# Kernel tuning notes

Measured on AMD Instinct MI355X. Metric: run time of the kernel, lower is better.

The kernel has to match this reference:

```python
import jax, jax.numpy as jnp
import numpy as np


def setup_inputs() -> dict:
    key = jax.random.key(0)
    k1, k2, k3 = jax.random.split(key, 3)
    B, S, H, D, W = 2, 2048, 16, 128, 4  # W = world_size (ring steps); k,v carry W*S total KV
    q = jax.random.normal(k1, (B, S, H, D), dtype=jnp.float32)
    k = jax.random.normal(k2, (B, W * S, H, D), dtype=jnp.float32)
    v = jax.random.normal(k3, (B, W * S, H, D), dtype=jnp.float32)
    return {"q": q, "k": k, "v": v}


def _ring_attention(q, k, v):
    # q: [B,S,H,D]; k,v: [B,W*S,H,D] -- W ring steps over KV chunks of length S
    B, S, H, D = q.shape
    W = k.shape[1] // S
    scale = D ** -0.5
    kc = k.reshape(B, W, S, H, D).transpose(1, 0, 2, 3, 4)  # [W,B,S,H,D]
    vc = v.reshape(B, W, S, H, D).transpose(1, 0, 2, 3, 4)
    o0 = jnp.zeros((B, H, S, D), q.dtype)
    l0 = jnp.zeros((B, H, S, 1), q.dtype)
    m0 = jnp.full((B, H, S, 1), -jnp.inf, q.dtype)

    def step(carry, kv):
        o, l, m = carry
        kb, vb = kv  # [B,S,H,D]
        scores = jnp.einsum('bqhd,bkhd->bhqk', q, kb) * scale  # [B,H,S,S]
        m_blk = jnp.max(scores, axis=-1, keepdims=True)
        p = jnp.exp(scores - m_blk)
        l_blk = jnp.sum(p, axis=-1, keepdims=True)
        m_new = jnp.maximum(m, m_blk)
        alpha = jnp.exp(m - m_blk * 0 - m_new) if False else jnp.exp(m - m_new)
        beta = jnp.exp(m_blk - m_new)
        l_new = alpha * l + beta * l_blk
        o_blk = jnp.einsum('bhqk,bkhd->bhqd', p, vb)
        o_new = (alpha * o * l + beta * o_blk) / l_new  # online-softmax rescale (same as torch code)
        return (o_new, l_new, m_new), None

    (o, l, m), _ = jax.lax.scan(step, (o0, l0, m0), (kc, vc))
    return o.transpose(0, 2, 1, 3)  # back to [B,S,H,D]


def reference(q, k, v):
    return _ring_attention(q, k, v)
```

## Files before the change

### kernel.cpp

```cpp
#include <hip/hip_runtime.h>

namespace {
constexpr int Bc  = 2;
constexpr int Sq  = 2048;
constexpr int Hn  = 16;
constexpr int Dd  = 128;
constexpr int Skv = 8192;
constexpr int TK  = 64;
constexpr int NT  = Skv / TK;
constexpr int QT  = 256;
constexpr int PP  = 72;
constexpr int TILE_ELEMS = TK * Dd;
constexpr int QTF = 128;
constexpr int KPF = 136;
constexpr float C_EXP = (float)(0.08838834764831845 * 1.4426950408889634);
}

typedef __attribute__((ext_vector_type(8))) short short8;
typedef __attribute__((ext_vector_type(8))) unsigned short us8;
typedef __attribute__((ext_vector_type(4))) float f32x4;
typedef __attribute__((ext_vector_type(4))) unsigned short us4;

__device__ __forceinline__ unsigned short f2bf(float f) {
  unsigned int u = __builtin_bit_cast(unsigned int, f);
  u += 0x7fffu + ((u >> 16) & 1u);
  return (unsigned short)(u >> 16);
}

__device__ __forceinline__ void gload16(const unsigned short* g, unsigned short* l) {
  __builtin_amdgcn_global_load_lds(
      (__attribute__((address_space(1))) void*)(g),
      (__attribute__((address_space(3))) void*)(l), 16, 0, 0);
}

__global__ __launch_bounds__(256) void convert_kernel(
    const float* __restrict__ kg, const float* __restrict__ vg,
    unsigned short* __restrict__ kws, unsigned short* __restrict__ vws) {
  const int t = threadIdx.x;
  const int bid = blockIdx.x;
  const int bh = bid >> 7;
  const int tile = bid & 127;
  const int b = bh >> 4, h = bh & (Hn - 1);
  const size_t HD = (size_t)Hn * Dd;

  const float* kin = kg + ((size_t)b * Skv + (size_t)tile * TK) * HD + (size_t)h * Dd;
  const float* vin = vg + ((size_t)b * Skv + (size_t)tile * TK) * HD + (size_t)h * Dd;
  unsigned short* kout = kws + (size_t)bid * TILE_ELEMS;
  unsigned short* vout = vws + (size_t)bid * TILE_ELEMS;

  {
    const int key = t >> 2;
    const float* krow = kin + (size_t)key * HD;
    unsigned short* orow = kout + key * Dd;
#pragma unroll
    for (int i = 0; i < 4; ++i) {
      const int dblk = (t & 3) * 4 + i;
      const int dsrc = dblk ^ (key & 7);
      float4 a = *(const float4*)(krow + dsrc * 8);
      float4 c = *(const float4*)(krow + dsrc * 8 + 4);
      us8 w;
      w[0] = f2bf(a.x); w[1] = f2bf(a.y); w[2] = f2bf(a.z); w[3] = f2bf(a.w);
      w[4] = f2bf(c.x); w[5] = f2bf(c.y); w[6] = f2bf(c.z); w[7] = f2bf(c.w);
      *(us8*)&orow[dblk * 8] = w;
    }
  }

  {
    const int kblk = t & 7;
    const int d4 = t >> 3;
#pragma unroll
    for (int eh = 0; eh < 2; ++eh) {
      const int f = (2 * d4 + eh) & 7;
      const int sb = kblk ^ f;
      us8 w0, w1;
#pragma unroll
      for (int r = 0; r < 8; ++r) {
        const float* vp = vin + (size_t)(sb * 8 + r) * HD + d4 * 4 + 2 * eh;
        float2 vv = *(const float2*)vp;
        w0[r] = f2bf(vv.x);
        w1[r] = f2bf(vv.y);
      }
      const int d0 = d4 * 4 + 2 * eh;
      *(us8*)&vout[d0 * TK + kblk * 8] = w0;
      *(us8*)&vout[(d0 + 1) * TK + kblk * 8] = w1;
    }
  }
}

__global__ __launch_bounds__(512, 2) void ring_attn_bf16(
    const float* __restrict__ qg, const unsigned short* __restrict__ kws,
    const unsigned short* __restrict__ vws, float* __restrict__ og) {
  __shared__ unsigned short lds_k[2][TK * Dd];
  __shared__ unsigned short lds_vt[2][Dd * TK];
  __shared__ unsigned short lds_p[8 * 32 * PP];

  const int t    = threadIdx.x;
  const int wave = t >> 6;
  const int lane = t & 63;
  const int l15  = lane & 15;
  const int quad = lane >> 4;
  const int bid  = blockIdx.x;
  const int bh = ((bid & 7) << 2) | (bid >> 6);
  const int qt = (bid >> 3) & 7;
  const int h  = bh & (Hn - 1);
  const int b  = bh >> 4;
  const size_t HD = (size_t)Hn * Dd;

  const unsigned short* kbh = kws + (size_t)bh * (NT * (size_t)TILE_ELEMS);
  const unsigned short* vbh = vws + (size_t)bh * (NT * (size_t)TILE_ELEMS);
  const int c0 = wave * 1024 + lane * 8;

#pragma unroll
  for (int j = 0; j < 2; ++j) {
    gload16(kbh + c0 + j * 512, &lds_k[0][wave * 1024 + j * 512]);
    gload16(vbh + c0 + j * 512, &lds_vt[0][wave * 1024 + j * 512]);
  }

  short8 qfrag[2][4];
  {
    const float* qbase = qg + ((size_t)b * Sq) * HD + (size_t)h * Dd;
#pragma unroll
    for (int mt = 0; mt < 2; ++mt) {
      const int qrow = qt * QT + wave * 32 + mt * 16 + l15;
      const float* qp = qbase + (size_t)qrow * HD;
#pragma unroll
      for (int kk = 0; kk < 4; ++kk) {
        const float* p8 = qp + kk * 32 + quad * 8;
        float4 a = *(const float4*)p8;
        float4 c = *(const float4*)(p8 + 4);
        short8 f;
        f[0] = (short)f2bf(a.x); f[1] = (short)f2bf(a.y);
        f[2] = (short)f2bf(a.z); f[3] = (short)f2bf(a.w);
        f[4] = (short)f2bf(c.x); f[5] = (short)f2bf(c.y);
        f[6] = (short)f2bf(c.z); f[7] = (short)f2bf(c.w);
        qfrag[mt][kk] = f;
      }
    }
  }

  f32x4 acco[2][8];
#pragma unroll
  for (int mt = 0; mt < 2; ++mt)
#pragma unroll
    for (int n = 0; n < 8; ++n)
      acco[mt][n] = (f32x4){0.f, 0.f, 0.f, 0.f};

  float l_part[2][4];
#pragma unroll
  for (int mt = 0; mt < 2; ++mt)
#pragma unroll
    for (int i = 0; i < 4; ++i) l_part[mt][i] = 0.f;

  int koff[4], voff[2];
#pragma unroll
  for (int kk = 0; kk < 4; ++kk) koff[kk] = ((kk * 4 + quad) ^ (l15 & 7)) * 8;
#pragma unroll
  for (int kk = 0; kk < 2; ++kk) voff[kk] = ((kk * 4 + quad) ^ ((l15 >> 1) & 7)) * 8;

  asm volatile("s_waitcnt vmcnt(0)" ::: "memory");
  __syncthreads();

  int buf = 0;
  for (int it = 0; it < NT; ++it) {
    if (it + 1 < NT) {
      const unsigned short* kt = kbh + (size_t)(it + 1) * TILE_ELEMS;
      const unsigned short* vt = vbh + (size_t)(it + 1) * TILE_ELEMS;
      unsigned short* kd = &lds_k[buf ^ 1][wave * 1024];
      unsigned short* vd = &lds_vt[buf ^ 1][wave * 1024];
#pragma unroll
      for (int j = 0; j < 2; ++j) {
        gload16(kt + c0 + j * 512, kd + j * 512);
        gload16(vt + c0 + j * 512, vd + j * 512);
      }
    }

    const unsigned short* kb = &lds_k[buf][0];
    f32x4 accs[2][4];
#pragma unroll
    for (int mt = 0; mt < 2; ++mt)
#pragma unroll
      for (int n = 0; n < 4; ++n)
        accs[mt][n] = (f32x4){0.f, 0.f, 0.f, 0.f};

    __builtin_amdgcn_s_setprio(1);
#pragma unroll
    for (int n = 0; n < 4; ++n) {
      short8 bfr[4];
#pragma unroll
      for (int kk = 0; kk < 4; ++kk)
        bfr[kk] = *(const short8*)&kb[(n * 16 + l15) * Dd + koff[kk]];
#pragma unroll
      for (int mt = 0; mt < 2; ++mt)
#pragma unroll
        for (int kk = 0; kk < 4; ++kk)
          accs[mt][n] = __builtin_amdgcn_mfma_f32_16x16x32_bf16(
              qfrag[mt][kk], bfr[kk], accs[mt][n], 0, 0, 0);
    }
    __builtin_amdgcn_s_setprio(0);

#pragma unroll
    for (int mt = 0; mt < 2; ++mt) {
#pragma unroll
      for (int i = 0; i < 4; ++i) {
        float s0 = __builtin_amdgcn_exp2f(accs[mt][0][i] * C_EXP);
        float s1 = __builtin_amdgcn_exp2f(accs[mt][1][i] * C_EXP);
        float s2 = __builtin_amdgcn_exp2f(accs[mt][2][i] * C_EXP);
        float s3 = __builtin_amdgcn_exp2f(accs[mt][3][i] * C_EXP);
        accs[mt][0][i] = s0; accs[mt][1][i] = s1;
        accs[mt][2][i] = s2; accs[mt][3][i] = s3;
        l_part[mt][i] += (s0 + s1) + (s2 + s3);
      }
#pragma unroll
      for (int n = 0; n < 4; ++n)
#pragma unroll
        for (int i = 0; i < 4; ++i)
          lds_p[wave * (32 * PP) + (mt * 16 + quad * 4 + i) * PP + n * 16 + l15] =
              f2bf(accs[mt][n][i]);
    }

    asm volatile("s_waitcnt lgkmcnt(0)" ::: "memory");

    const unsigned short* vb = &lds_vt[buf][0];
    __builtin_amdgcn_s_setprio(1);
#pragma unroll
    for (int kk = 0; kk < 2; ++kk) {
      short8 afr[2];
#pragma unroll
      for (int mt = 0; mt < 2; ++mt)
        afr[mt] = *(const short8*)&lds_p[wave * (32 * PP) + (mt * 16 + l15) * PP +
                                         kk * 32 + quad * 8];
#pragma unroll
      for (int n = 0; n < 8; ++n) {
        short8 bfr = *(const short8*)&vb[(n * 16 + l15) * TK + voff[kk]];
        acco[0][n] = __builtin_amdgcn_mfma_f32_16x16x32_bf16(afr[0], bfr, acco[0][n], 0, 0, 0);
        acco[1][n] = __builtin_amdgcn_mfma_f32_16x16x32_bf16(afr[1], bfr, acco[1][n], 0, 0, 0);
      }
    }
    __builtin_amdgcn_s_setprio(0);

    asm volatile("s_waitcnt vmcnt(0)" ::: "memory");
    __syncthreads();
    buf ^= 1;
  }

#pragma unroll
  for (int mt = 0; mt < 2; ++mt)
#pragma unroll
    for (int i = 0; i < 4; ++i) {
      float l = l_part[mt][i];
#pragma unroll
      for (int off = 1; off < 16; off <<= 1) l += __shfl_xor(l, off);
      l_part[mt][i] = l;
    }

  float* ob = og + ((size_t)b * Sq) * HD + (size_t)h * Dd;
#pragma unroll
  for (int mt = 0; mt < 2; ++mt) {
#pragma unroll
    for (int i = 0; i < 4; ++i) {
      const int qrow = qt * QT + wave * 32 + mt * 16 + quad * 4 + i;
      const float inv = 1.0f / l_part[mt][i];
      float* op = ob + (size_t)qrow * HD;
#pragma unroll
      for (int n = 0; n < 8; ++n)
        op[n * 16 + l15] = acco[mt][n][i] * inv;
    }
  }
}

__global__ __launch_bounds__(256) void ring_attn_fallback(
    const float* __restrict__ qg, const float* __restrict__ kg,
    const float* __restrict__ vg, float* __restrict__ og) {
  __shared__ unsigned short lds_k[TK * KPF];
  __shared__ unsigned short lds_vt[Dd * 64];
  __shared__ unsigned short lds_p[4 * 32 * PP];

  const int t    = threadIdx.x;
  const int wave = t >> 6;
  const int lane = t & 63;
  const int l15  = lane & 15;
  const int quad = lane >> 4;
  const int bid  = blockIdx.x;
  const int bh = ((bid & 7) << 2) | (bid >> 7);
  const int qt = (bid >> 3) & 15;
  const int h  = bh & (Hn - 1);
  const int b  = bh >> 4;
  const size_t HD = (size_t)Hn * Dd;

  short8 qfrag[2][4];
  {
    const float* qbase = qg + ((size_t)b * Sq) * HD + (size_t)h * Dd;
    for (int mt = 0; mt < 2; ++mt) {
      const int qrow = qt * QTF + wave * 32 + mt * 16 + l15;
      const float* qp = qbase + (size_t)qrow * HD;
#pragma unroll
      for (int kk = 0; kk < 4; ++kk) {
        const float* p8 = qp + kk * 32 + quad * 8;
        float4 a = *(const float4*)p8;
        float4 c = *(const float4*)(p8 + 4);
        short8 f;
        f[0] = (short)f2bf(a.x); f[1] = (short)f2bf(a.y);
        f[2] = (short)f2bf(a.z); f[3] = (short)f2bf(a.w);
        f[4] = (short)f2bf(c.x); f[5] = (short)f2bf(c.y);
        f[6] = (short)f2bf(c.z); f[7] = (short)f2bf(c.w);
        qfrag[mt][kk] = f;
      }
    }
  }

  f32x4 acco[2][8];
#pragma unroll
  for (int mt = 0; mt < 2; ++mt)
#pragma unroll
    for (int n = 0; n < 8; ++n)
      acco[mt][n] = (f32x4){0.f, 0.f, 0.f, 0.f};

  float l_part[2][4];
#pragma unroll
  for (int mt = 0; mt < 2; ++mt)
#pragma unroll
    for (int i = 0; i < 4; ++i) l_part[mt][i] = 0.f;

  const float* kb_g = kg + ((size_t)b * Skv) * HD + (size_t)h * Dd;
  const float* vb_g = vg + ((size_t)b * Skv) * HD + (size_t)h * Dd;
  const int th = t >> 5;
  const int tl = t & 31;
  const int dq = tl << 2;

  for (int it = 0; it < Skv / TK; ++it) {
    const int kv0 = it * TK;
    __syncthreads();

#pragma unroll
    for (int r = 0; r < 8; ++r) {
      const int key = th + r * 8;
      float4 k4 = *(const float4*)(kb_g + (size_t)(kv0 + key) * HD + dq);
      us4 kw;
      kw[0] = f2bf(k4.x); kw[1] = f2bf(k4.y);
      kw[2] = f2bf(k4.z); kw[3] = f2bf(k4.w);
      *(us4*)&lds_k[key * KPF + dq] = kw;
    }

    {
      const int vK0 = th << 3;
      us4 vreg[8];
#pragma unroll
      for (int r = 0; r < 8; ++r) {
        float4 v4 = *(const float4*)(vb_g + (size_t)(kv0 + vK0 + r) * HD + dq);
        vreg[r][0] = f2bf(v4.x); vreg[r][1] = f2bf(v4.y);
        vreg[r][2] = f2bf(v4.z); vreg[r][3] = f2bf(v4.w);
      }
      const int kbp = (th ^ (tl & 7)) << 3;
#pragma unroll
      for (int i = 0; i < 4; ++i) {
        const int d = dq + i;
        us8 w;
#pragma unroll
        for (int r = 0; r < 8; ++r) w[r] = vreg[r][i];
        *(us8*)&lds_vt[d * 64 + kbp] = w;
      }
    }
    __syncthreads();

    f32x4 accs[2][4];
#pragma unroll
    for (int mt = 0; mt < 2; ++mt)
#pragma unroll
      for (int n = 0; n < 4; ++n)
        accs[mt][n] = (f32x4){0.f, 0.f, 0.f, 0.f};

#pragma unroll
    for (int n = 0; n < 4; ++n) {
      short8 bfr[4];
#pragma unroll
      for (int kk = 0; kk < 4; ++kk)
        bfr[kk] = *(const short8*)&lds_k[(n * 16 + l15) * KPF + kk * 32 + quad * 8];
#pragma unroll
      for (int mt = 0; mt < 2; ++mt)
#pragma unroll
        for (int kk = 0; kk < 4; ++kk)
          accs[mt][n] = __builtin_amdgcn_mfma_f32_16x16x32_bf16(
              qfrag[mt][kk], bfr[kk], accs[mt][n], 0, 0, 0);
    }

#pragma unroll
    for (int mt = 0; mt < 2; ++mt) {
#pragma unroll
      for (int i = 0; i < 4; ++i) {
        float s0 = __builtin_amdgcn_exp2f(accs[mt][0][i] * C_EXP);
        float s1 = __builtin_amdgcn_exp2f(accs[mt][1][i] * C_EXP);
        float s2 = __builtin_amdgcn_exp2f(accs[mt][2][i] * C_EXP);
        float s3 = __builtin_amdgcn_exp2f(accs[mt][3][i] * C_EXP);
        accs[mt][0][i] = s0; accs[mt][1][i] = s1;
        accs[mt][2][i] = s2; accs[mt][3][i] = s3;
        l_part[mt][i] += (s0 + s1) + (s2 + s3);
      }
#pragma unroll
      for (int n = 0; n < 4; ++n)
#pragma unroll
        for (int i = 0; i < 4; ++i)
          lds_p[wave * (32 * PP) + (mt * 16 + quad * 4 + i) * PP + n * 16 + l15] =
              f2bf(accs[mt][n][i]);
    }

    asm volatile("s_waitcnt lgkmcnt(0)" ::: "memory");

#pragma unroll
    for (int kk = 0; kk < 2; ++kk) {
      short8 afr[2];
#pragma unroll
      for (int mt = 0; mt < 2; ++mt)
        afr[mt] = *(const short8*)&lds_p[wave * (32 * PP) + (mt * 16 + l15) * PP +
                                         kk * 32 + quad * 8];
#pragma unroll
      for (int n = 0; n < 8; ++n) {
        const int dcol = n * 16 + l15;
        const int kbr = ((quad + 4 * kk) ^ ((dcol >> 2) & 7)) << 3;
        short8 bfr = *(const short8*)&lds_vt[dcol * 64 + kbr];
        acco[0][n] = __builtin_amdgcn_mfma_f32_16x16x32_bf16(afr[0], bfr, acco[0][n], 0, 0, 0);
        acco[1][n] = __builtin_amdgcn_mfma_f32_16x16x32_bf16(afr[1], bfr, acco[1][n], 0, 0, 0);
      }
    }
  }

#pragma unroll
  for (int mt = 0; mt < 2; ++mt)
#pragma unroll
    for (int i = 0; i < 4; ++i) {
      float l = l_part[mt][i];
#pragma unroll
      for (int off = 1; off < 16; off <<= 1) l += __shfl_xor(l, off);
      l_part[mt][i] = l;
    }

  float* ob = og + ((size_t)b * Sq) * HD + (size_t)h * Dd;
#pragma unroll
  for (int mt = 0; mt < 2; ++mt) {
#pragma unroll
    for (int i = 0; i < 4; ++i) {
      const int qrow = qt * QTF + wave * 32 + mt * 16 + quad * 4 + i;
      const float inv = 1.0f / l_part[mt][i];
      float* op = ob + (size_t)qrow * HD;
#pragma unroll
      for (int n = 0; n < 8; ++n)
        op[n * 16 + l15] = acco[mt][n][i] * inv;
    }
  }
}

extern "C" void kernel_launch(void* const* d_in, const int* in_sizes, int n_in,
                              void* d_out, int out_size, void* d_ws, size_t ws_size,
                              hipStream_t stream) {
  const float* q = (const float*)d_in[0];
  const float* k = (const float*)d_in[1];
  const float* v = (const float*)d_in[2];
  float* out = (float*)d_out;

  constexpr size_t KWS_ELEMS = (size_t)Bc * Hn * NT * TILE_ELEMS;
  constexpr size_t WS_NEED = 2 * KWS_ELEMS * sizeof(unsigned short);

  if (d_ws != nullptr && ws_size >= WS_NEED) {
    unsigned short* kws = (unsigned short*)d_ws;
    unsigned short* vws = kws + KWS_ELEMS;
    convert_kernel<<<dim3(Bc * Hn * NT), dim3(256), 0, stream>>>(k, v, kws, vws);
    ring_attn_bf16<<<dim3(Bc * Hn * (Sq / QT)), dim3(512), 0, stream>>>(q, kws, vws, out);
  } else {
    ring_attn_fallback<<<dim3(Bc * Hn * (Sq / QTF)), dim3(256), 0, stream>>>(q, k, v, out);
  }
}
```

Before: 673.9 us.

## Transpose S MFMA operands for vectorized P stores and stage V transpose via LDS

```diff
diff --git a/kernel.cpp b/kernel.cpp
--- a/kernel.cpp
+++ b/kernel.cpp
@@ -10,6 +10,7 @@
 constexpr int NT  = Skv / TK;
 constexpr int QT  = 256;
 constexpr int PP  = 72;
+constexpr int PV  = 132;
 constexpr int TILE_ELEMS = TK * Dd;
 constexpr int QTF = 128;
 constexpr int KPF = 136;
@@ -36,6 +37,8 @@
 __global__ __launch_bounds__(256) void convert_kernel(
     const float* __restrict__ kg, const float* __restrict__ vg,
     unsigned short* __restrict__ kws, unsigned short* __restrict__ vws) {
+  __shared__ unsigned short lds_v[TK * PV];
+
   const int t = threadIdx.x;
   const int bid = blockIdx.x;
   const int bh = bid >> 7;
@@ -50,6 +53,20 @@
 
   {
     const int key = t >> 2;
+    const int c   = t & 3;
+    const float* vrow = vin + (size_t)key * HD + c * 32;
+    unsigned short* lrow = &lds_v[key * PV + c * 32];
+#pragma unroll
+    for (int j = 0; j < 8; ++j) {
+      float4 a = *(const float4*)(vrow + 4 * j);
+      us4 w;
+      w[0] = f2bf(a.x); w[1] = f2bf(a.y); w[2] = f2bf(a.z); w[3] = f2bf(a.w);
+      *(us4*)&lrow[4 * j] = w;
+    }
+  }
+
+  {
+    const int key = t >> 2;
     const float* krow = kin + (size_t)key * HD;
     unsigned short* orow = kout + key * Dd;
 #pragma unroll
@@ -57,32 +74,28 @@
       const int dblk = (t & 3) * 4 + i;
       const int dsrc = dblk ^ (key & 7);
       float4 a = *(const float4*)(krow + dsrc * 8);
-      float4 c = *(const float4*)(krow + dsrc * 8 + 4);
+      float4 c4 = *(const float4*)(krow + dsrc * 8 + 4);
       us8 w;
-      w[0] = f2bf(a.x); w[1] = f2bf(a.y); w[2] = f2bf(a.z); w[3] = f2bf(a.w);
-      w[4] = f2bf(c.x); w[5] = f2bf(c.y); w[6] = f2bf(c.z); w[7] = f2bf(c.w);
+      w[0] = f2bf(a.x);  w[1] = f2bf(a.y);  w[2] = f2bf(a.z);  w[3] = f2bf(a.w);
+      w[4] = f2bf(c4.x); w[5] = f2bf(c4.y); w[6] = f2bf(c4.z); w[7] = f2bf(c4.w);
       *(us8*)&orow[dblk * 8] = w;
     }
   }
 
+  __syncthreads();
+
   {
-    const int kblk = t & 7;
-    const int d4 = t >> 3;
-#pragma unroll
-    for (int eh = 0; eh < 2; ++eh) {
-      const int f = (2 * d4 + eh) & 7;
-      const int sb = kblk ^ f;
-      us8 w0, w1;
-#pragma unroll
-      for (int r = 0; r < 8; ++r) {
-        const float* vp = vin + (size_t)(sb * 8 + r) * HD + d4 * 4 + 2 * eh;
-        float2 vv = *(const float2*)vp;
-        w0[r] = f2bf(vv.x);
-        w1[r] = f2bf(vv.y);
-      }
-      const int d0 = d4 * 4 + 2 * eh;
-      *(us8*)&vout[d0 * TK + kblk * 8] = w0;
-      *(us8*)&vout[(d0 + 1) * TK + kblk * 8] = w1;
+    const int d = t >> 1;
+    const int half = t & 1;
+    const int f = (d >> 1) & 7;
+#pragma unroll
+    for (int jj = 0; jj < 4; ++jj) {
+      const int kp = half * 4 + jj;
+      const int sb = kp ^ f;
+      us8 w;
+#pragma unroll
+      for (int r = 0; r < 8; ++r) w[r] = lds_v[(sb * 8 + r) * PV + d];
+      *(us8*)&vout[d * TK + kp * 8] = w;
     }
   }
 }
@@ -145,11 +158,7 @@
     for (int n = 0; n < 8; ++n)
       acco[mt][n] = (f32x4){0.f, 0.f, 0.f, 0.f};
 
-  float l_part[2][4];
-#pragma unroll
-  for (int mt = 0; mt < 2; ++mt)
-#pragma unroll
-    for (int i = 0; i < 4; ++i) l_part[mt][i] = 0.f;
+  float l_part[2] = {0.f, 0.f};
 
   int koff[4], voff[2];
 #pragma unroll
@@ -194,28 +203,25 @@
 #pragma unroll
         for (int kk = 0; kk < 4; ++kk)
           accs[mt][n] = __builtin_amdgcn_mfma_f32_16x16x32_bf16(
-              qfrag[mt][kk], bfr[kk], accs[mt][n], 0, 0, 0);
+              bfr[kk], qfrag[mt][kk], accs[mt][n], 0, 0, 0);
     }
     __builtin_amdgcn_s_setprio(0);
 
 #pragma unroll
     for (int mt = 0; mt < 2; ++mt) {
-#pragma unroll
-      for (int i = 0; i < 4; ++i) {
-        float s0 = __builtin_amdgcn_exp2f(accs[mt][0][i] * C_EXP);
-        float s1 = __builtin_amdgcn_exp2f(accs[mt][1][i] * C_EXP);
-        float s2 = __builtin_amdgcn_exp2f(accs[mt][2][i] * C_EXP);
-        float s3 = __builtin_amdgcn_exp2f(accs[mt][3][i] * C_EXP);
-        accs[mt][0][i] = s0; accs[mt][1][i] = s1;
-        accs[mt][2][i] = s2; accs[mt][3][i] = s3;
-        l_part[mt][i] += (s0 + s1) + (s2 + s3);
-      }
-#pragma unroll
-      for (int n = 0; n < 4; ++n)
-#pragma unroll
-        for (int i = 0; i < 4; ++i)
-          lds_p[wave * (32 * PP) + (mt * 16 + quad * 4 + i) * PP + n * 16 + l15] =
-              f2bf(accs[mt][n][i]);
+      float lacc = 0.f;
+#pragma unroll
+      for (int n = 0; n < 4; ++n) {
+        float s0 = __builtin_amdgcn_exp2f(accs[mt][n][0] * C_EXP);
+        float s1 = __builtin_amdgcn_exp2f(accs[mt][n][1] * C_EXP);
+        float s2 = __builtin_amdgcn_exp2f(accs[mt][n][2] * C_EXP);
+        float s3 = __builtin_amdgcn_exp2f(accs[mt][n][3] * C_EXP);
+        lacc += (s0 + s1) + (s2 + s3);
+        us4 w;
+        w[0] = f2bf(s0); w[1] = f2bf(s1); w[2] = f2bf(s2); w[3] = f2bf(s3);
+        *(us4*)&lds_p[wave * (32 * PP) + (mt * 16 + l15) * PP + n * 16 + quad * 4] = w;
+      }
+      l_part[mt] += lacc;
     }
 
     asm volatile("s_waitcnt lgkmcnt(0)" ::: "memory");
@@ -244,14 +250,12 @@
   }
 
 #pragma unroll
-  for (int mt = 0; mt < 2; ++mt)
-#pragma unroll
-    for (int i = 0; i < 4; ++i) {
-      float l = l_part[mt][i];
-#pragma unroll
-      for (int off = 1; off < 16; off <<= 1) l += __shfl_xor(l, off);
-      l_part[mt][i] = l;
-    }
+  for (int mt = 0; mt < 2; ++mt) {
+    float l = l_part[mt];
+    l += __shfl_xor(l, 16);
+    l += __shfl_xor(l, 32);
+    l_part[mt] = l;
+  }
 
   float* ob = og + ((size_t)b * Sq) * HD + (size_t)h * Dd;
 #pragma unroll
@@ -259,7 +263,7 @@
 #pragma unroll
     for (int i = 0; i < 4; ++i) {
       const int qrow = qt * QT + wave * 32 + mt * 16 + quad * 4 + i;
-      const float inv = 1.0f / l_part[mt][i];
+      const float inv = 1.0f / __shfl(l_part[mt], quad * 4 + i);
       float* op = ob + (size_t)qrow * HD;
 #pragma unroll
       for (int n = 0; n < 8; ++n)
```

Result: faster. 660.7 us (-2.0%).
